# Optimization experiments

Measured on AMD Instinct MI355X. Metric: run time of the kernel, lower is better.

Reference implementation:

```python
import jax, jax.numpy as jnp
import numpy as np

EPS_BN = 1e-3   # nn.BatchNorm1d(eps=0.001)
LAMDA = 1e-5    # Point_Attentation.lamda


def _bn(x, g, b, m, v):
    # inference-mode BatchNorm1d over last dim
    return (x - m) * (g * jax.lax.rsqrt(v + EPS_BN)) + b


def _forward(features_low, features_high,
             bott_W, bott_b, bott_gamma, bott_beta, bott_mean, bott_var,
             qkv_W, qkv_gamma, qkv_beta, qkv_mean, qkv_var,
             mlp_W, mlp_gamma, mlp_beta, mlp_mean, mlp_var,
             fus_W, fus_b, fus_gamma, fus_beta, fus_mean, fus_var,
             batch_size):
    N, C = features_low.shape
    B = batch_size
    n = N // B  # points per batch segment (equal-length segments)

    # ---- Point_Attentation: per-point channel mean, var over channels / (n-1) ----
    x = features_low
    mean = jnp.mean(x, axis=-1, keepdims=True)
    d = x - mean
    var = jnp.sum(d * d, axis=-1, keepdims=True) / (n - 1)
    e_t = d * d / (4.0 * (var + LAMDA)) + 0.5
    x = x + jax.nn.sigmoid(e_t) * x

    for i in range(3):
        y = jax.nn.relu(_bn(x @ bott_W[2 * i] + bott_b[2 * i],
                            bott_gamma[2 * i], bott_beta[2 * i], bott_mean[2 * i], bott_var[2 * i]))
        y = jax.nn.relu(_bn(y @ bott_W[2 * i + 1] + bott_b[2 * i + 1],
                            bott_gamma[2 * i + 1], bott_beta[2 * i + 1], bott_mean[2 * i + 1], bott_var[2 * i + 1]))
        x = x + y

    # ---- fusion: per-batch QKV attention between low (x) and high features ----
    low = x.reshape(B, n, C)
    high = features_high.reshape(B, n, C)

    q = _bn(jnp.einsum('bnc,cd->bnd', low, qkv_W[0]), qkv_gamma[0], qkv_beta[0], qkv_mean[0], qkv_var[0])
    k = _bn(jnp.einsum('bnc,cd->bnd', high, qkv_W[1]), qkv_gamma[1], qkv_beta[1], qkv_mean[1], qkv_var[1])
    v = _bn(jnp.einsum('bnc,cd->bnd', high, qkv_W[2]), qkv_gamma[2], qkv_beta[2], qkv_mean[2], qkv_var[2])

    scale = 1.0 / jnp.sqrt(jnp.asarray(256.0, dtype=q.dtype))  # normal_dim = 256
    attn = jax.nn.softmax(jnp.einsum('bqc,bkc->bqk', q, k) * scale, axis=-1)
    ao = jnp.einsum('bqk,bkc->bqc', attn, v)

    # mlp: (Linear no-bias -> BN -> Dropout(eval=id) -> ReLU) x2
    h = jax.nn.relu(_bn(jnp.einsum('bnc,cd->bnd', ao, mlp_W[0]), mlp_gamma[0], mlp_beta[0], mlp_mean[0], mlp_var[0]))
    h = jax.nn.relu(_bn(jnp.einsum('bnc,cd->bnd', h, mlp_W[1]), mlp_gamma[1], mlp_beta[1], mlp_mean[1], mlp_var[1]))

    # linear_fusion: Linear(2C->C, bias) -> BN -> ReLU
    cat = jnp.concatenate([low, h], axis=-1)  # [B, n, 2C]
    out = jax.nn.relu(_bn(jnp.einsum('bnc,cd->bnd', cat, fus_W) + fus_b, fus_gamma, fus_beta, fus_mean, fus_var))
    return out.reshape(N, C)


def setup_inputs() -> dict:
    key = jax.random.key(0)
    ks = jax.random.split(key, 16)
    N, C, B = 16384, 256, 4
    s = 0.05
    d = {}
    d['features_low'] = jax.random.normal(ks[0], (N, C), jnp.float32)
    d['features_high'] = jax.random.normal(ks[1], (N, C), jnp.float32)
    d['bott_W'] = jax.random.normal(ks[2], (6, C, C), jnp.float32) * s
    d['bott_b'] = jnp.zeros((6, C), jnp.float32)
    d['bott_gamma'] = jnp.ones((6, C), jnp.float32)
    d['bott_beta'] = jnp.zeros((6, C), jnp.float32)
    d['bott_mean'] = jnp.zeros((6, C), jnp.float32)
    d['bott_var'] = jnp.ones((6, C), jnp.float32)
    d['qkv_W'] = jax.random.normal(ks[3], (3, C, C), jnp.float32) * s
    d['qkv_gamma'] = jnp.ones((3, C), jnp.float32)
    d['qkv_beta'] = jnp.zeros((3, C), jnp.float32)
    d['qkv_mean'] = jnp.zeros((3, C), jnp.float32)
    d['qkv_var'] = jnp.ones((3, C), jnp.float32)
    d['mlp_W'] = jax.random.normal(ks[4], (2, C, C), jnp.float32) * s
    d['mlp_gamma'] = jnp.ones((2, C), jnp.float32)
    d['mlp_beta'] = jnp.zeros((2, C), jnp.float32)
    d['mlp_mean'] = jnp.zeros((2, C), jnp.float32)
    d['mlp_var'] = jnp.ones((2, C), jnp.float32)
    d['fus_W'] = jax.random.normal(ks[5], (2 * C, C), jnp.float32) * s
    d['fus_b'] = jnp.zeros((C,), jnp.float32)
    d['fus_gamma'] = jnp.ones((C,), jnp.float32)
    d['fus_beta'] = jnp.zeros((C,), jnp.float32)
    d['fus_mean'] = jnp.zeros((C,), jnp.float32)
    d['fus_var'] = jnp.ones((C,), jnp.float32)
    d['batch_size'] = B
    return d


def reference(features_low, features_high,
              bott_W, bott_b, bott_gamma, bott_beta, bott_mean, bott_var,
              qkv_W, qkv_gamma, qkv_beta, qkv_mean, qkv_var,
              mlp_W, mlp_gamma, mlp_beta, mlp_mean, mlp_var,
              fus_W, fus_b, fus_gamma, fus_beta, fus_mean, fus_var,
              batch_size):
    return _forward(features_low, features_high,
                    bott_W, bott_b, bott_gamma, bott_beta, bott_mean, bott_var,
                    qkv_W, qkv_gamma, qkv_beta, qkv_mean, qkv_var,
                    mlp_W, mlp_gamma, mlp_beta, mlp_mean, mlp_var,
                    fus_W, fus_b, fus_gamma, fus_beta, fus_mean, fus_var,
                    batch_size)
```

## Files before the change

kernel.cpp:

```cpp
#include <hip/hip_runtime.h>
#include <cstdint>
#include <cstddef>

typedef float v4f __attribute__((ext_vector_type(4)));
typedef float v2f __attribute__((ext_vector_type(2)));
typedef short v8s __attribute__((ext_vector_type(8)));
typedef unsigned short v4u __attribute__((ext_vector_type(4)));

typedef unsigned short ubf;

#define NPTS 16384
#define CD   256
#define NBAT 4
#define NPB  4096

__device__ __forceinline__ float bf2f(ubf u) {
    union { unsigned u; float f; } c; c.u = ((unsigned)u) << 16; return c.f;
}
__device__ __forceinline__ ubf f2bf(float f) {
    union { float f; unsigned u; } c; c.f = f;
    unsigned u = c.u;
    u += 0x7fffu + ((u >> 16) & 1u);
    return (ubf)(u >> 16);
}

__global__ __launch_bounds__(256) void k_pre(
    const float* __restrict__ low, float* __restrict__ xout,
    const float* __restrict__ bott, const float* __restrict__ qkv,
    const float* __restrict__ mlp, const float* __restrict__ fus,
    ubf* __restrict__ wt) {
    const int bid = blockIdx.x;
    if (bid < 4096) {
        const int lane = threadIdx.x & 63;
        const int row  = bid * 4 + (threadIdx.x >> 6);
        const float* p = low + (size_t)row * CD + lane * 4;
        v4f v = *reinterpret_cast<const v4f*>(p);
        float d[4];
        float s = v[0] + v[1] + v[2] + v[3];
#pragma unroll
        for (int o = 32; o >= 1; o >>= 1) s += __shfl_xor(s, o);
        const float mean = s * (1.0f / 256.0f);
        float ss = 0.f;
#pragma unroll
        for (int i = 0; i < 4; ++i) { d[i] = v[i] - mean; ss += d[i] * d[i]; }
#pragma unroll
        for (int o = 32; o >= 1; o >>= 1) ss += __shfl_xor(ss, o);
        const float var = ss * (1.0f / 4095.0f);
        const float dn  = 1.0f / (4.0f * (var + 1e-5f));
        v4f o;
#pragma unroll
        for (int i = 0; i < 4; ++i) {
            const float e   = d[i] * d[i] * dn + 0.5f;
            const float sig = 1.0f / (1.0f + __expf(-e));
            o[i] = v[i] * (1.0f + sig);
        }
        *reinterpret_cast<v4f*>(xout + (size_t)row * CD + lane * 4) = o;
        return;
    }
    const int bid2 = bid - 4096;
    const int z = bid2 >> 7, r = bid2 & 127;
    const float* src; int K; size_t doff;
    if (z < 6)       { src = bott + (size_t)z * 65536;       K = 256; doff = (size_t)z * 65536; }
    else if (z < 9)  { src = qkv  + (size_t)(z - 6) * 65536; K = 256; doff = (size_t)z * 65536; }
    else if (z < 11) { src = mlp  + (size_t)(z - 9) * 65536; K = 256; doff = (size_t)z * 65536; }
    else             { src = fus;                            K = 512; doff = (size_t)11 * 65536; }
    const int kt = (r >> 3) * 32, nt = (r & 7) * 32;
    if (kt >= K) return;
    __shared__ ubf tile[32][33];
    const int tx = threadIdx.x & 31, ty = threadIdx.x >> 5;
#pragma unroll
    for (int i = 0; i < 4; ++i)
        tile[ty * 4 + i][tx] = f2bf(src[(size_t)(kt + ty * 4 + i) * 256 + nt + tx]);
    __syncthreads();
    ubf* dst = wt + doff;
#pragma unroll
    for (int i = 0; i < 4; ++i)
        dst[(size_t)(nt + ty * 4 + i) * K + kt + tx] = tile[tx][ty * 4 + i];
}

__global__ __launch_bounds__(256) void k_conv1(
    float* __restrict__ xA, const ubf* __restrict__ wT,
    const float* __restrict__ bb, const float* __restrict__ bg,
    const float* __restrict__ bbe, const float* __restrict__ bm_,
    const float* __restrict__ bv) {
    __shared__ __attribute__((aligned(16))) float xls[64 * 256];
    __shared__ __attribute__((aligned(16))) ubf   yls[64 * 256];

    const int lane = threadIdx.x & 63;
    const int w    = threadIdx.x >> 6;
    const int wr = w >> 1, wc = w & 1;
    const int q15 = lane & 15, g = lane >> 4;
    const int bm = blockIdx.x * 64;

    {
        float* xsrcb = xA + (size_t)bm * 256;
#pragma unroll
        for (int it = 0; it < 16; ++it) {
            const int L4 = (it * 256 + w * 64) * 4;
            const int Ll = L4 + lane * 4;
            const int row = Ll >> 8, col = (Ll & 255) ^ ((row & 7) << 3);
            __builtin_amdgcn_global_load_lds(
                (const __attribute__((address_space(1))) unsigned*)(xsrcb + row * 256 + col),
                (__attribute__((address_space(3))) unsigned*)(xls + L4), 16, 0, 0);
        }
    }
    __syncthreads();

    const int r0l = wr * 32 + q15;
#pragma unroll 1
    for (int s = 0; s < 3; ++s) {
        const ubf* W0 = wT + (size_t)(2 * s) * 65536;
        const ubf* W1 = wT + (size_t)(2 * s + 1) * 65536;

        v4f acc[2][8];
#pragma unroll
        for (int i = 0; i < 2; ++i)
#pragma unroll
            for (int j = 0; j < 8; ++j)
#pragma unroll
                for (int r = 0; r < 4; ++r) acc[i][j][r] = 0.f;
        for (int ks = 0; ks < 8; ++ks) {
            const int k0 = ks * 32 + g * 8;
            v8s afr[2], bfr[8];
#pragma unroll
            for (int mi = 0; mi < 2; ++mi) {
                const int row = r0l + mi * 16;
                const float* ap = &xls[row * 256 + (k0 ^ ((row & 7) << 3))];
                v4f a = *reinterpret_cast<const v4f*>(ap);
                v4f b = *reinterpret_cast<const v4f*>(ap + 4);
                v8s t;
#pragma unroll
                for (int j = 0; j < 4; ++j) { t[j] = (short)f2bf(a[j]); t[j + 4] = (short)f2bf(b[j]); }
                afr[mi] = t;
            }
#pragma unroll
            for (int ni = 0; ni < 8; ++ni)
                bfr[ni] = *reinterpret_cast<const v8s*>(W0 + (size_t)(wc * 128 + ni * 16 + q15) * 256 + k0);
#pragma unroll
            for (int mi = 0; mi < 2; ++mi)
#pragma unroll
                for (int ni = 0; ni < 8; ++ni)
                    acc[mi][ni] = __builtin_amdgcn_mfma_f32_16x16x32_bf16(afr[mi], bfr[ni], acc[mi][ni], 0, 0, 0);
        }
#pragma unroll
        for (int ni = 0; ni < 8; ++ni) {
            const int col = wc * 128 + ni * 16 + q15;
            const float sc  = bg[2 * s * 256 + col] * rsqrtf(bv[2 * s * 256 + col] + 1e-3f);
            const float tc  = bbe[2 * s * 256 + col] - bm_[2 * s * 256 + col] * sc;
            const float bia = bb[2 * s * 256 + col];
#pragma unroll
            for (int mi = 0; mi < 2; ++mi)
#pragma unroll
                for (int r = 0; r < 4; ++r) {
                    const int row = wr * 32 + mi * 16 + g * 4 + r;
                    float z = (acc[mi][ni][r] + bia) * sc + tc;
                    z = fmaxf(z, 0.f);
                    yls[row * 256 + (col ^ ((row & 7) << 3))] = f2bf(z);
                }
        }
        __syncthreads();

#pragma unroll
        for (int i = 0; i < 2; ++i)
#pragma unroll
            for (int j = 0; j < 8; ++j)
#pragma unroll
                for (int r = 0; r < 4; ++r) acc[i][j][r] = 0.f;
        for (int ks = 0; ks < 8; ++ks) {
            const int k0 = ks * 32 + g * 8;
            v8s afr[2], bfr[8];
#pragma unroll
            for (int mi = 0; mi < 2; ++mi) {
                const int row = r0l + mi * 16;
                afr[mi] = *reinterpret_cast<const v8s*>(&yls[row * 256 + (k0 ^ ((row & 7) << 3))]);
            }
#pragma unroll
            for (int ni = 0; ni < 8; ++ni)
                bfr[ni] = *reinterpret_cast<const v8s*>(W1 + (size_t)(wc * 128 + ni * 16 + q15) * 256 + k0);
#pragma unroll
            for (int mi = 0; mi < 2; ++mi)
#pragma unroll
                for (int ni = 0; ni < 8; ++ni)
                    acc[mi][ni] = __builtin_amdgcn_mfma_f32_16x16x32_bf16(afr[mi], bfr[ni], acc[mi][ni], 0, 0, 0);
        }
#pragma unroll
        for (int ni = 0; ni < 8; ++ni) {
            const int col = wc * 128 + ni * 16 + q15;
            const int c1 = (2 * s + 1) * 256 + col;
            const float sc  = bg[c1] * rsqrtf(bv[c1] + 1e-3f);
            const float tc  = bbe[c1] - bm_[c1] * sc;
            const float bia = bb[c1];
#pragma unroll
            for (int mi = 0; mi < 2; ++mi)
#pragma unroll
                for (int r = 0; r < 4; ++r) {
                    const int row = wr * 32 + mi * 16 + g * 4 + r;
                    float z = (acc[mi][ni][r] + bia) * sc + tc;
                    z = fmaxf(z, 0.f);
                    xls[row * 256 + (col ^ ((row & 7) << 3))] += z;
                }
        }
        __syncthreads();
    }

    {
        float* xdstb = xA + (size_t)bm * 256;
#pragma unroll
        for (int it = 0; it < 16; ++it) {
            const int Ll = (it * 256 + threadIdx.x) * 4;
            const int row = Ll >> 8, cl = Ll & 255;
            const int gcol = cl ^ ((row & 7) << 3);
            *reinterpret_cast<v4f*>(xdstb + row * 256 + gcol) =
                *reinterpret_cast<const v4f*>(xls + Ll);
        }
    }
}

__global__ __launch_bounds__(256) void k_qkv(
    const float* __restrict__ xA, const float* __restrict__ fh,
    const ubf* __restrict__ wTq,
    const float* __restrict__ qg, const float* __restrict__ qbe,
    const float* __restrict__ qm, const float* __restrict__ qv,
    ubf* __restrict__ qB, ubf* __restrict__ kB, ubf* __restrict__ vT) {
    const int m = blockIdx.y >> 1;
    const float* Af = (m == 0) ? xA : fh;
    const ubf* WT = wTq + m * 65536;
    const float* gamma = qg + m * 256;
    const float* beta  = qbe + m * 256;
    const float* bmean = qm + m * 256;
    const float* bvar  = qv + m * 256;

    const int lane = threadIdx.x & 63;
    const int w    = threadIdx.x >> 6;
    const int wr = w >> 1, wc = w & 1;
    const int q15 = lane & 15, g = lane >> 4;
    const int bm = blockIdx.x * 128, bn = (blockIdx.y & 1) * 128;
    const int r0 = bm + wr * 64 + q15;
    const int c0 = bn + wc * 64 + q15;

    v4f acc[4][4];
#pragma unroll
    for (int i = 0; i < 4; ++i)
#pragma unroll
        for (int j = 0; j < 4; ++j)
#pragma unroll
            for (int r = 0; r < 4; ++r) acc[i][j][r] = 0.f;

    for (int ks = 0; ks < 8; ++ks) {
        const int k0 = ks * 32 + g * 8;
        v8s afr[4], bfr[4];
#pragma unroll
        for (int mi = 0; mi < 4; ++mi) {
            const float* ap = Af + (size_t)(r0 + mi * 16) * CD + k0;
            v4f a = *reinterpret_cast<const v4f*>(ap);
            v4f b = *reinterpret_cast<const v4f*>(ap + 4);
            v8s t;
#pragma unroll
            for (int j = 0; j < 4; ++j) { t[j] = (short)f2bf(a[j]); t[j + 4] = (short)f2bf(b[j]); }
            afr[mi] = t;
        }
#pragma unroll
        for (int ni = 0; ni < 4; ++ni)
            bfr[ni] = *reinterpret_cast<const v8s*>(WT + (size_t)(c0 + ni * 16) * 256 + k0);
#pragma unroll
        for (int mi = 0; mi < 4; ++mi)
#pragma unroll
            for (int ni = 0; ni < 4; ++ni)
                acc[mi][ni] = __builtin_amdgcn_mfma_f32_16x16x32_bf16(afr[mi], bfr[ni], acc[mi][ni], 0, 0, 0);
    }

    ubf* outb = (m == 0) ? qB : kB;
#pragma unroll
    for (int ni = 0; ni < 4; ++ni) {
        const int col = c0 + ni * 16;
        const float sc = gamma[col] * rsqrtf(bvar[col] + 1e-3f);
        const float tc = beta[col] - bmean[col] * sc;
#pragma unroll
        for (int mi = 0; mi < 4; ++mi) {
            if (m == 2) {
                const int row0 = bm + wr * 64 + mi * 16 + g * 4;
                v4u pk;
#pragma unroll
                for (int r = 0; r < 4; ++r) pk[r] = f2bf(acc[mi][ni][r] * sc + tc);
                const int bb = row0 >> 12, key = row0 & 4095;
                *reinterpret_cast<v4u*>(vT + ((size_t)(bb * CD + col)) * NPB + key) = pk;
            } else {
#pragma unroll
                for (int r = 0; r < 4; ++r) {
                    const int row = bm + wr * 64 + mi * 16 + g * 4 + r;
                    outb[(size_t)row * CD + col] = f2bf(acc[mi][ni][r] * sc + tc);
                }
            }
        }
    }
}

__device__ __forceinline__ void stage_k256(const ubf* __restrict__ kg,
                                           ubf* kd, int wave, int lane) {
#pragma unroll
    for (int it = 0; it < 8; ++it) {
        const int Lb = it * 2048 + wave * 512;
        const int L  = Lb + lane * 8;
        const int key = L >> 8, c8 = (L & 255) ^ ((key & 7) << 3);
        __builtin_amdgcn_global_load_lds(
            (const __attribute__((address_space(1))) unsigned*)(kg + key * CD + c8),
            (__attribute__((address_space(3))) unsigned*)(kd + Lb), 16, 0, 0);
    }
}
__device__ __forceinline__ void stage_v256(const ubf* __restrict__ vg,
                                           ubf* vd, int wave, int lane) {
#pragma unroll
    for (int it = 0; it < 8; ++it) {
        const int Lb = it * 2048 + wave * 512;
        const int L  = Lb + lane * 8;
        const int c = L >> 6, k8 = (L & 63) ^ ((c & 7) << 3);
        __builtin_amdgcn_global_load_lds(
            (const __attribute__((address_space(1))) unsigned*)(vg + (size_t)c * NPB + k8),
            (__attribute__((address_space(3))) unsigned*)(vd + Lb), 16, 0, 0);
    }
}

__global__ __launch_bounds__(256) void k_attn(const ubf* __restrict__ qb, const ubf* __restrict__ kb,
                                              const ubf* __restrict__ vt,
                                              ubf* __restrict__ o0, ubf* __restrict__ o1,
                                              float* __restrict__ ml) {
    __shared__ __attribute__((aligned(16))) ubf kls[64 * 256];
    __shared__ __attribute__((aligned(16))) ubf vls[256 * 64];
    __shared__ __attribute__((aligned(16))) ubf pls[4 * 16 * 64];

    const int raw = blockIdx.x;
    const int xcd = raw & 7, qt = raw >> 3;
    const int b = xcd >> 1, half = xcd & 1;

    const int wave = threadIdx.x >> 6, lane = threadIdx.x & 63;
    const int q15 = lane & 15, g = lane >> 4;

    const ubf* qrow = qb + ((size_t)(b * NPB + qt * 64 + wave * 16 + q15)) * CD + g * 8;
    v8s qf[8];
#pragma unroll
    for (int cs = 0; cs < 8; ++cs) qf[cs] = *reinterpret_cast<const v8s*>(qrow + cs * 32);

    v4f oacc[16];
#pragma unroll
    for (int i = 0; i < 16; ++i)
#pragma unroll
        for (int r = 0; r < 4; ++r) oacc[i][r] = 0.f;
    float m_run = -3.0e38f, l_run = 0.f;

    const ubf* kgb = kb + ((size_t)(b * NPB) + half * 2048) * CD;
    const ubf* vgb = vt + (size_t)b * CD * NPB + half * 2048;
    ubf* pw = pls + wave * 1024;

    stage_k256(kgb, kls, wave, lane);
    __syncthreads();

    for (int kc = 0; kc < 32; ++kc) {
        stage_v256(vgb + kc * 64, vls, wave, lane);

        v4f sacc[4];
#pragma unroll
        for (int f = 0; f < 4; ++f)
#pragma unroll
            for (int r = 0; r < 4; ++r) sacc[f][r] = 0.f;
#pragma unroll
        for (int cs = 0; cs < 8; ++cs)
#pragma unroll
            for (int f = 0; f < 4; ++f) {
                const int key = 16 * f + q15;
                v8s af = *reinterpret_cast<const v8s*>(&kls[(key * CD + cs * 32 + g * 8) ^ ((key & 7) << 3)]);
                sacc[f] = __builtin_amdgcn_mfma_f32_16x16x32_bf16(af, qf[cs], sacc[f], 0, 0, 0);
            }

        __syncthreads();
        if (kc + 1 < 32)
            stage_k256(kgb + (size_t)(kc + 1) * 64 * CD, kls, wave, lane);

        float mloc = -3.0e38f;
#pragma unroll
        for (int f = 0; f < 4; ++f)
#pragma unroll
            for (int r = 0; r < 4; ++r) {
                float x = sacc[f][r] * 0.0625f;
                sacc[f][r] = x;
                mloc = fmaxf(mloc, x);
            }
        mloc = fmaxf(mloc, __shfl_xor(mloc, 16));
        mloc = fmaxf(mloc, __shfl_xor(mloc, 32));
        if (!__all(mloc <= m_run + 8.0f)) {
            const float mnew  = fmaxf(m_run, mloc);
            const float alpha = __expf(m_run - mnew);
            l_run *= alpha;
#pragma unroll
            for (int i = 0; i < 16; ++i)
#pragma unroll
                for (int r = 0; r < 4; ++r) oacc[i][r] *= alpha;
            m_run = mnew;
        }
        float lloc = 0.f;
#pragma unroll
        for (int f = 0; f < 4; ++f)
#pragma unroll
            for (int r = 0; r < 4; ++r) {
                float p = __expf(sacc[f][r] - m_run);
                sacc[f][r] = p;
                lloc += p;
            }
        lloc += __shfl_xor(lloc, 16);
        lloc += __shfl_xor(lloc, 32);
        l_run += lloc;

#pragma unroll
        for (int f = 0; f < 4; ++f) {
            unsigned u0, u1, u2, u3;
            { union { float f; unsigned u; } c; c.f = sacc[f][0]; u0 = c.u; }
            { union { float f; unsigned u; } c; c.f = sacc[f][1]; u1 = c.u; }
            { union { float f; unsigned u; } c; c.f = sacc[f][2]; u2 = c.u; }
            { union { float f; unsigned u; } c; c.f = sacc[f][3]; u3 = c.u; }
            unsigned p01 = (u0 >> 16) | (u1 & 0xFFFF0000u);
            unsigned p23 = (u2 >> 16) | (u3 & 0xFFFF0000u);
            const int e = q15 * 64 + 16 * f + 4 * g;
            *reinterpret_cast<unsigned*>(&pw[(e)     ^ ((q15 & 7) << 3)]) = p01;
            *reinterpret_cast<unsigned*>(&pw[(e + 2) ^ ((q15 & 7) << 3)]) = p23;
        }
        v8s pb0 = *reinterpret_cast<const v8s*>(&pw[(q15 * 64 +  0 + 8 * g) ^ ((q15 & 7) << 3)]);
        v8s pb1 = *reinterpret_cast<const v8s*>(&pw[(q15 * 64 + 32 + 8 * g) ^ ((q15 & 7) << 3)]);
#pragma unroll
        for (int mt = 0; mt < 16; ++mt) {
            const int c = 16 * mt + q15;
            v8s av0 = *reinterpret_cast<const v8s*>(&vls[(c * 64 +  0 + 8 * g) ^ ((c & 7) << 3)]);
            oacc[mt] = __builtin_amdgcn_mfma_f32_16x16x32_bf16(av0, pb0, oacc[mt], 0, 0, 0);
            v8s av1 = *reinterpret_cast<const v8s*>(&vls[(c * 64 + 32 + 8 * g) ^ ((c & 7) << 3)]);
            oacc[mt] = __builtin_amdgcn_mfma_f32_16x16x32_bf16(av1, pb1, oacc[mt], 0, 0, 0);
        }

        __syncthreads();
    }

    const int grow = b * NPB + qt * 64 + wave * 16 + q15;
    ubf* aor = (half ? o1 : o0) + (size_t)grow * CD;
#pragma unroll
    for (int mt = 0; mt < 16; ++mt) {
        v4u pk;
#pragma unroll
        for (int r = 0; r < 4; ++r) pk[r] = f2bf(oacc[mt][r]);
        *reinterpret_cast<v4u*>(aor + 16 * mt + 4 * g) = pk;
    }
    if (g == 0) {
        v2f d; d[0] = m_run; d[1] = l_run;
        *reinterpret_cast<v2f*>(ml + (size_t)(half * NPTS + grow) * 2) = d;
    }
}

__global__ __launch_bounds__(256) void k_tail(
    const ubf* __restrict__ o0, const ubf* __restrict__ o1, const float* __restrict__ ml,
    const float* __restrict__ xA, const ubf* __restrict__ wT,
    const float* __restrict__ mg, const float* __restrict__ mbe,
    const float* __restrict__ mm, const float* __restrict__ mv,
    const float* __restrict__ fb, const float* __restrict__ fg,
    const float* __restrict__ fbe, const float* __restrict__ fm,
    const float* __restrict__ fv, float* __restrict__ out) {
    __shared__ __attribute__((aligned(16))) ubf yls[64 * 256];

    const int lane = threadIdx.x & 63;
    const int w    = threadIdx.x >> 6;
    const int wr = w >> 1, wc = w & 1;
    const int q15 = lane & 15, g = lane >> 4;
    const int bm = blockIdx.x * 64;
    const int r0l = wr * 32 + q15;

    const ubf* W9  = wT + (size_t)9 * 65536;
    const ubf* W10 = wT + (size_t)10 * 65536;
    const ubf* W11 = wT + (size_t)11 * 65536;

    v4f acc[2][8];

    float a0[2], a1[2];
#pragma unroll
    for (int mi = 0; mi < 2; ++mi) {
        const int row = bm + r0l + mi * 16;
        const float m0 = ml[2 * row],          l0 = ml[2 * row + 1];
        const float m1 = ml[2 * (NPTS + row)], l1 = ml[2 * (NPTS + row) + 1];
        const float mx = fmaxf(m0, m1);
        const float w0 = __expf(m0 - mx), w1 = __expf(m1 - mx);
        const float inv = 1.0f / (w0 * l0 + w1 * l1);
        a0[mi] = w0 * inv; a1[mi] = w1 * inv;
    }
#pragma unroll
    for (int i = 0; i < 2; ++i)
#pragma unroll
        for (int j = 0; j < 8; ++j)
#pragma unroll
            for (int r = 0; r < 4; ++r) acc[i][j][r] = 0.f;
    for (int ks = 0; ks < 8; ++ks) {
        const int k0 = ks * 32 + g * 8;
        v8s afr[2], bfr[8];
#pragma unroll
        for (int mi = 0; mi < 2; ++mi) {
            const int row = bm + r0l + mi * 16;
            v8s u0 = *reinterpret_cast<const v8s*>(o0 + (size_t)row * CD + k0);
            v8s u1 = *reinterpret_cast<const v8s*>(o1 + (size_t)row * CD + k0);
            v8s t;
#pragma unroll
            for (int j = 0; j < 8; ++j)
                t[j] = (short)f2bf(a0[mi] * bf2f((ubf)u0[j]) + a1[mi] * bf2f((ubf)u1[j]));
            afr[mi] = t;
        }
#pragma unroll
        for (int ni = 0; ni < 8; ++ni)
            bfr[ni] = *reinterpret_cast<const v8s*>(W9 + (size_t)(wc * 128 + ni * 16 + q15) * 256 + k0);
#pragma unroll
        for (int mi = 0; mi < 2; ++mi)
#pragma unroll
            for (int ni = 0; ni < 8; ++ni)
                acc[mi][ni] = __builtin_amdgcn_mfma_f32_16x16x32_bf16(afr[mi], bfr[ni], acc[mi][ni], 0, 0, 0);
    }
#pragma unroll
    for (int ni = 0; ni < 8; ++ni) {
        const int col = wc * 128 + ni * 16 + q15;
        const float sc = mg[col] * rsqrtf(mv[col] + 1e-3f);
        const float tc = mbe[col] - mm[col] * sc;
#pragma unroll
        for (int mi = 0; mi < 2; ++mi)
#pragma unroll
            for (int r = 0; r < 4; ++r) {
                const int row = wr * 32 + mi * 16 + g * 4 + r;
                float z = fmaxf(acc[mi][ni][r] * sc + tc, 0.f);
                yls[row * 256 + (col ^ ((row & 7) << 3))] = f2bf(z);
            }
    }
    __syncthreads();

#pragma unroll
    for (int i = 0; i < 2; ++i)
#pragma unroll
        for (int j = 0; j < 8; ++j)
#pragma unroll
            for (int r = 0; r < 4; ++r) acc[i][j][r] = 0.f;
    for (int ks = 0; ks < 8; ++ks) {
        const int k0 = ks * 32 + g * 8;
        v8s afr[2], bfr[8];
#pragma unroll
        for (int mi = 0; mi < 2; ++mi) {
            const int row = r0l + mi * 16;
            afr[mi] = *reinterpret_cast<const v8s*>(&yls[row * 256 + (k0 ^ ((row & 7) << 3))]);
        }
#pragma unroll
        for (int ni = 0; ni < 8; ++ni)
            bfr[ni] = *reinterpret_cast<const v8s*>(W10 + (size_t)(wc * 128 + ni * 16 + q15) * 256 + k0);
#pragma unroll
        for (int mi = 0; mi < 2; ++mi)
#pragma unroll
            for (int ni = 0; ni < 8; ++ni)
                acc[mi][ni] = __builtin_amdgcn_mfma_f32_16x16x32_bf16(afr[mi], bfr[ni], acc[mi][ni], 0, 0, 0);
    }
    __syncthreads();
#pragma unroll
    for (int ni = 0; ni < 8; ++ni) {
        const int col = wc * 128 + ni * 16 + q15;
        const float sc = mg[256 + col] * rsqrtf(mv[256 + col] + 1e-3f);
        const float tc = mbe[256 + col] - mm[256 + col] * sc;
#pragma unroll
        for (int mi = 0; mi < 2; ++mi)
#pragma unroll
            for (int r = 0; r < 4; ++r) {
                const int row = wr * 32 + mi * 16 + g * 4 + r;
                float z = fmaxf(acc[mi][ni][r] * sc + tc, 0.f);
                yls[row * 256 + (col ^ ((row & 7) << 3))] = f2bf(z);
            }
    }
    __syncthreads();

#pragma unroll
    for (int i = 0; i < 2; ++i)
#pragma unroll
        for (int j = 0; j < 8; ++j)
#pragma unroll
            for (int r = 0; r < 4; ++r) acc[i][j][r] = 0.f;
    for (int ks = 0; ks < 16; ++ks) {
        const int k0 = ks * 32 + g * 8;
        v8s afr[2], bfr[8];
#pragma unroll
        for (int mi = 0; mi < 2; ++mi) {
            if (k0 < 256) {
                const float* ap = xA + (size_t)(bm + r0l + mi * 16) * CD + k0;
                v4f a = *reinterpret_cast<const v4f*>(ap);
                v4f b = *reinterpret_cast<const v4f*>(ap + 4);
                v8s t;
#pragma unroll
                for (int j = 0; j < 4; ++j) { t[j] = (short)f2bf(a[j]); t[j + 4] = (short)f2bf(b[j]); }
                afr[mi] = t;
            } else {
                const int row = r0l + mi * 16, kk = k0 - 256;
                afr[mi] = *reinterpret_cast<const v8s*>(&yls[row * 256 + (kk ^ ((row & 7) << 3))]);
            }
        }
#pragma unroll
        for (int ni = 0; ni < 8; ++ni)
            bfr[ni] = *reinterpret_cast<const v8s*>(W11 + (size_t)(wc * 128 + ni * 16 + q15) * 512 + k0);
#pragma unroll
        for (int mi = 0; mi < 2; ++mi)
#pragma unroll
            for (int ni = 0; ni < 8; ++ni)
                acc[mi][ni] = __builtin_amdgcn_mfma_f32_16x16x32_bf16(afr[mi], bfr[ni], acc[mi][ni], 0, 0, 0);
    }
#pragma unroll
    for (int ni = 0; ni < 8; ++ni) {
        const int col = wc * 128 + ni * 16 + q15;
        const float sc = fg[col] * rsqrtf(fv[col] + 1e-3f);
        const float tc = fbe[col] - fm[col] * sc;
        const float bia = fb[col];
#pragma unroll
        for (int mi = 0; mi < 2; ++mi)
#pragma unroll
            for (int r = 0; r < 4; ++r) {
                const int row = bm + wr * 32 + mi * 16 + g * 4 + r;
                float z = fmaxf((acc[mi][ni][r] + bia) * sc + tc, 0.f);
                out[(size_t)row * CD + col] = z;
            }
    }
}

extern "C" void kernel_launch(void* const* d_in, const int* in_sizes, int n_in,
                              void* d_out, int out_size, void* d_ws, size_t ws_size,
                              hipStream_t stream) {
    const float* f_low   = (const float*)d_in[0];
    const float* f_high  = (const float*)d_in[1];
    const float* bott_W  = (const float*)d_in[2];
    const float* bott_b  = (const float*)d_in[3];
    const float* bott_g  = (const float*)d_in[4];
    const float* bott_be = (const float*)d_in[5];
    const float* bott_m  = (const float*)d_in[6];
    const float* bott_v  = (const float*)d_in[7];
    const float* qkv_W   = (const float*)d_in[8];
    const float* qkv_g   = (const float*)d_in[9];
    const float* qkv_be  = (const float*)d_in[10];
    const float* qkv_m   = (const float*)d_in[11];
    const float* qkv_v   = (const float*)d_in[12];
    const float* mlp_W   = (const float*)d_in[13];
    const float* mlp_g   = (const float*)d_in[14];
    const float* mlp_be  = (const float*)d_in[15];
    const float* mlp_m   = (const float*)d_in[16];
    const float* mlp_v   = (const float*)d_in[17];
    const float* fus_W   = (const float*)d_in[18];
    const float* fus_b   = (const float*)d_in[19];
    const float* fus_g   = (const float*)d_in[20];
    const float* fus_be  = (const float*)d_in[21];
    const float* fus_m   = (const float*)d_in[22];
    const float* fus_v   = (const float*)d_in[23];
    (void)in_sizes; (void)n_in; (void)out_size; (void)ws_size;

    char* ws = (char*)d_ws;
    const size_t MB = 1024 * 1024;
    float* xA = (float*)(ws);
    ubf*   o0 = (ubf*)  (ws + 17 * MB);
    ubf*   qB = (ubf*)  (ws + 26 * MB);
    ubf*   kB = (ubf*)  (ws + 35 * MB);
    ubf*   vT = (ubf*)  (ws + 44 * MB);
    ubf*   wT = (ubf*)  (ws + 53 * MB);
    ubf*   o1 = (ubf*)  (ws + 56 * MB);
    float* ml = (float*)(ws + 65 * MB);

    k_pre<<<dim3(4096 + 1536), dim3(256), 0, stream>>>(f_low, xA,
                                                       bott_W, qkv_W, mlp_W, fus_W, wT);

    k_conv1<<<dim3(256), dim3(256), 0, stream>>>(xA, wT,
                                                 bott_b, bott_g, bott_be, bott_m, bott_v);

    k_qkv<<<dim3(128, 6), dim3(256), 0, stream>>>(xA, f_high, wT + (size_t)6 * 65536,
                                                  qkv_g, qkv_be, qkv_m, qkv_v, qB, kB, vT);

    k_attn<<<dim3(512), dim3(256), 0, stream>>>(qB, kB, vT, o0, o1, ml);

    k_tail<<<dim3(256), dim3(256), 0, stream>>>(o0, o1, ml, xA, wT,
                                                mlp_g, mlp_be, mlp_m, mlp_v,
                                                fus_b, fus_g, fus_be, fus_m, fus_v,
                                                (float*)d_out);
}
```

Measured before the change: 305.3 us.

## Merge conv1 with K/V projection, split Q projection, double attention query tile

The bottleneck stack and the K/V projections now share one heterogeneous launch. Conv1 uses 32-row tiles over 512 blocks, and the remaining 512 blocks compute K and V from features_high, which does not depend on conv1. Q projection becomes its own kernel. The attention kernel now gives each wave two 16-row query sub-tiles, halving grid size and reusing each staged K/V tile across twice as many queries, at the cost of higher register pressure (launch_bounds 256,1).

```diff
diff --git a/kernel.cpp b/kernel.cpp
--- a/kernel.cpp
+++ b/kernel.cpp
@@ -78,165 +78,208 @@
         dst[(size_t)(nt + ty * 4 + i) * K + kt + tx] = tile[tx][ty * 4 + i];
 }
 
-__global__ __launch_bounds__(256) void k_conv1(
-    float* __restrict__ xA, const ubf* __restrict__ wT,
+__global__ __launch_bounds__(256) void k_mid(
+    float* __restrict__ xA, const float* __restrict__ fh, const ubf* __restrict__ wT,
     const float* __restrict__ bb, const float* __restrict__ bg,
     const float* __restrict__ bbe, const float* __restrict__ bm_,
-    const float* __restrict__ bv) {
-    __shared__ __attribute__((aligned(16))) float xls[64 * 256];
-    __shared__ __attribute__((aligned(16))) ubf   yls[64 * 256];
+    const float* __restrict__ bv,
+    const float* __restrict__ qg, const float* __restrict__ qbe,
+    const float* __restrict__ qm, const float* __restrict__ qv,
+    ubf* __restrict__ kB, ubf* __restrict__ vT) {
+    __shared__ __attribute__((aligned(16))) float xls[32 * 256];
+    __shared__ __attribute__((aligned(16))) ubf   yls[32 * 256];
 
     const int lane = threadIdx.x & 63;
     const int w    = threadIdx.x >> 6;
     const int wr = w >> 1, wc = w & 1;
     const int q15 = lane & 15, g = lane >> 4;
-    const int bm = blockIdx.x * 64;
-
-    {
-        float* xsrcb = xA + (size_t)bm * 256;
-#pragma unroll
-        for (int it = 0; it < 16; ++it) {
-            const int L4 = (it * 256 + w * 64) * 4;
-            const int Ll = L4 + lane * 4;
-            const int row = Ll >> 8, col = (Ll & 255) ^ ((row & 7) << 3);
-            __builtin_amdgcn_global_load_lds(
-                (const __attribute__((address_space(1))) unsigned*)(xsrcb + row * 256 + col),
-                (__attribute__((address_space(3))) unsigned*)(xls + L4), 16, 0, 0);
-        }
-    }
-    __syncthreads();
-
-    const int r0l = wr * 32 + q15;
+    const int bid = blockIdx.x;
+
+    if (bid < 512) {
+        const int bm = bid * 32;
+        {
+            float* xsrcb = xA + (size_t)bm * 256;
+#pragma unroll
+            for (int it = 0; it < 8; ++it) {
+                const int L4 = (it * 256 + w * 64) * 4;
+                const int Ll = L4 + lane * 4;
+                const int row = Ll >> 8, col = (Ll & 255) ^ ((row & 7) << 3);
+                __builtin_amdgcn_global_load_lds(
+                    (const __attribute__((address_space(1))) unsigned*)(xsrcb + row * 256 + col),
+                    (__attribute__((address_space(3))) unsigned*)(xls + L4), 16, 0, 0);
+            }
+        }
+        __syncthreads();
+
+        const int r0l = wr * 16 + q15;
 #pragma unroll 1
-    for (int s = 0; s < 3; ++s) {
-        const ubf* W0 = wT + (size_t)(2 * s) * 65536;
-        const ubf* W1 = wT + (size_t)(2 * s + 1) * 65536;
-
-        v4f acc[2][8];
-#pragma unroll
-        for (int i = 0; i < 2; ++i)
+        for (int s = 0; s < 3; ++s) {
+            const ubf* W0 = wT + (size_t)(2 * s) * 65536;
+            const ubf* W1 = wT + (size_t)(2 * s + 1) * 65536;
+
+            v4f acc[8];
 #pragma unroll
             for (int j = 0; j < 8; ++j)
 #pragma unroll
-                for (int r = 0; r < 4; ++r) acc[i][j][r] = 0.f;
-        for (int ks = 0; ks < 8; ++ks) {
-            const int k0 = ks * 32 + g * 8;
-            v8s afr[2], bfr[8];
-#pragma unroll
-            for (int mi = 0; mi < 2; ++mi) {
-                const int row = r0l + mi * 16;
-                const float* ap = &xls[row * 256 + (k0 ^ ((row & 7) << 3))];
+                for (int r = 0; r < 4; ++r) acc[j][r] = 0.f;
+            for (int ks = 0; ks < 8; ++ks) {
+                const int k0 = ks * 32 + g * 8;
+                const float* ap = &xls[r0l * 256 + (k0 ^ ((r0l & 7) << 3))];
                 v4f a = *reinterpret_cast<const v4f*>(ap);
                 v4f b = *reinterpret_cast<const v4f*>(ap + 4);
-                v8s t;
-#pragma unroll
-                for (int j = 0; j < 4; ++j) { t[j] = (short)f2bf(a[j]); t[j + 4] = (short)f2bf(b[j]); }
-                afr[mi] = t;
-            }
-#pragma unroll
-            for (int ni = 0; ni < 8; ++ni)
-                bfr[ni] = *reinterpret_cast<const v8s*>(W0 + (size_t)(wc * 128 + ni * 16 + q15) * 256 + k0);
-#pragma unroll
-            for (int mi = 0; mi < 2; ++mi)
+                v8s afr;
+#pragma unroll
+                for (int j = 0; j < 4; ++j) { afr[j] = (short)f2bf(a[j]); afr[j + 4] = (short)f2bf(b[j]); }
+                v8s bfr[8];
 #pragma unroll
                 for (int ni = 0; ni < 8; ++ni)
-                    acc[mi][ni] = __builtin_amdgcn_mfma_f32_16x16x32_bf16(afr[mi], bfr[ni], acc[mi][ni], 0, 0, 0);
-        }
-#pragma unroll
-        for (int ni = 0; ni < 8; ++ni) {
-            const int col = wc * 128 + ni * 16 + q15;
-            const float sc  = bg[2 * s * 256 + col] * rsqrtf(bv[2 * s * 256 + col] + 1e-3f);
-            const float tc  = bbe[2 * s * 256 + col] - bm_[2 * s * 256 + col] * sc;
-            const float bia = bb[2 * s * 256 + col];
-#pragma unroll
-            for (int mi = 0; mi < 2; ++mi)
+                    bfr[ni] = *reinterpret_cast<const v8s*>(W0 + (size_t)(wc * 128 + ni * 16 + q15) * 256 + k0);
+#pragma unroll
+                for (int ni = 0; ni < 8; ++ni)
+                    acc[ni] = __builtin_amdgcn_mfma_f32_16x16x32_bf16(afr, bfr[ni], acc[ni], 0, 0, 0);
+            }
+#pragma unroll
+            for (int ni = 0; ni < 8; ++ni) {
+                const int col = wc * 128 + ni * 16 + q15;
+                const int c0i = 2 * s * 256 + col;
+                const float sc  = bg[c0i] * rsqrtf(bv[c0i] + 1e-3f);
+                const float tc  = bbe[c0i] - bm_[c0i] * sc;
+                const float bia = bb[c0i];
 #pragma unroll
                 for (int r = 0; r < 4; ++r) {
-                    const int row = wr * 32 + mi * 16 + g * 4 + r;
-                    float z = (acc[mi][ni][r] + bia) * sc + tc;
-                    z = fmaxf(z, 0.f);
+                    const int row = wr * 16 + g * 4 + r;
+                    float z = fmaxf((acc[ni][r] + bia) * sc + tc, 0.f);
                     yls[row * 256 + (col ^ ((row & 7) << 3))] = f2bf(z);
                 }
-        }
-        __syncthreads();
-
-#pragma unroll
-        for (int i = 0; i < 2; ++i)
+            }
+            __syncthreads();
+
 #pragma unroll
             for (int j = 0; j < 8; ++j)
 #pragma unroll
-                for (int r = 0; r < 4; ++r) acc[i][j][r] = 0.f;
-        for (int ks = 0; ks < 8; ++ks) {
-            const int k0 = ks * 32 + g * 8;
-            v8s afr[2], bfr[8];
-#pragma unroll
-            for (int mi = 0; mi < 2; ++mi) {
-                const int row = r0l + mi * 16;
-                afr[mi] = *reinterpret_cast<const v8s*>(&yls[row * 256 + (k0 ^ ((row & 7) << 3))]);
-            }
-#pragma unroll
-            for (int ni = 0; ni < 8; ++ni)
-                bfr[ni] = *reinterpret_cast<const v8s*>(W1 + (size_t)(wc * 128 + ni * 16 + q15) * 256 + k0);
-#pragma unroll
-            for (int mi = 0; mi < 2; ++mi)
+                for (int r = 0; r < 4; ++r) acc[j][r] = 0.f;
+            for (int ks = 0; ks < 8; ++ks) {
+                const int k0 = ks * 32 + g * 8;
+                v8s afr = *reinterpret_cast<const v8s*>(&yls[r0l * 256 + (k0 ^ ((r0l & 7) << 3))]);
+                v8s bfr[8];
 #pragma unroll
                 for (int ni = 0; ni < 8; ++ni)
-                    acc[mi][ni] = __builtin_amdgcn_mfma_f32_16x16x32_bf16(afr[mi], bfr[ni], acc[mi][ni], 0, 0, 0);
-        }
-#pragma unroll
-        for (int ni = 0; ni < 8; ++ni) {
-            const int col = wc * 128 + ni * 16 + q15;
-            const int c1 = (2 * s + 1) * 256 + col;
-            const float sc  = bg[c1] * rsqrtf(bv[c1] + 1e-3f);
-            const float tc  = bbe[c1] - bm_[c1] * sc;
-            const float bia = bb[c1];
-#pragma unroll
-            for (int mi = 0; mi < 2; ++mi)
+                    bfr[ni] = *reinterpret_cast<const v8s*>(W1 + (size_t)(wc * 128 + ni * 16 + q15) * 256 + k0);
+#pragma unroll
+                for (int ni = 0; ni < 8; ++ni)
+                    acc[ni] = __builtin_amdgcn_mfma_f32_16x16x32_bf16(afr, bfr[ni], acc[ni], 0, 0, 0);
+            }
+#pragma unroll
+            for (int ni = 0; ni < 8; ++ni) {
+                const int col = wc * 128 + ni * 16 + q15;
+                const int c1i = (2 * s + 1) * 256 + col;
+                const float sc  = bg[c1i] * rsqrtf(bv[c1i] + 1e-3f);
+                const float tc  = bbe[c1i] - bm_[c1i] * sc;
+                const float bia = bb[c1i];
 #pragma unroll
                 for (int r = 0; r < 4; ++r) {
-                    const int row = wr * 32 + mi * 16 + g * 4 + r;
-                    float z = (acc[mi][ni][r] + bia) * sc + tc;
-                    z = fmaxf(z, 0.f);
+                    const int row = wr * 16 + g * 4 + r;
+                    float z = fmaxf((acc[ni][r] + bia) * sc + tc, 0.f);
                     xls[row * 256 + (col ^ ((row & 7) << 3))] += z;
                 }
-        }
-        __syncthreads();
-    }
-
-    {
-        float* xdstb = xA + (size_t)bm * 256;
-#pragma unroll
-        for (int it = 0; it < 16; ++it) {
-            const int Ll = (it * 256 + threadIdx.x) * 4;
-            const int row = Ll >> 8, cl = Ll & 255;
-            const int gcol = cl ^ ((row & 7) << 3);
-            *reinterpret_cast<v4f*>(xdstb + row * 256 + gcol) =
-                *reinterpret_cast<const v4f*>(xls + Ll);
-        }
-    }
-}
-
-__global__ __launch_bounds__(256) void k_qkv(
-    const float* __restrict__ xA, const float* __restrict__ fh,
-    const ubf* __restrict__ wTq,
+            }
+            __syncthreads();
+        }
+
+        {
+            float* xdstb = xA + (size_t)bm * 256;
+#pragma unroll
+            for (int it = 0; it < 8; ++it) {
+                const int Ll = (it * 256 + threadIdx.x) * 4;
+                const int row = Ll >> 8, cl = Ll & 255;
+                *reinterpret_cast<v4f*>(xdstb + row * 256 + (cl ^ ((row & 7) << 3))) =
+                    *reinterpret_cast<const v4f*>(xls + Ll);
+            }
+        }
+        return;
+    }
+
+    const int bid2 = bid - 512;
+    const int m = bid2 >> 8;
+    const int sub = bid2 & 255;
+    const int bm = (sub >> 1) * 128, bn = (sub & 1) * 128;
+    const ubf* WT = wT + (size_t)(7 + m) * 65536;
+    const float* gamma = qg  + (1 + m) * 256;
+    const float* beta  = qbe + (1 + m) * 256;
+    const float* bmean = qm  + (1 + m) * 256;
+    const float* bvar  = qv  + (1 + m) * 256;
+    const int r0 = bm + wr * 64 + q15;
+    const int c0 = bn + wc * 64 + q15;
+
+    v4f acc[4][4];
+#pragma unroll
+    for (int i = 0; i < 4; ++i)
+#pragma unroll
+        for (int j = 0; j < 4; ++j)
+#pragma unroll
+            for (int r = 0; r < 4; ++r) acc[i][j][r] = 0.f;
+
+    for (int ks = 0; ks < 8; ++ks) {
+        const int k0 = ks * 32 + g * 8;
+        v8s afr[4], bfr[4];
+#pragma unroll
+        for (int mi = 0; mi < 4; ++mi) {
+            const float* ap = fh + (size_t)(r0 + mi * 16) * CD + k0;
+            v4f a = *reinterpret_cast<const v4f*>(ap);
+            v4f b = *reinterpret_cast<const v4f*>(ap + 4);
+            v8s t;
+#pragma unroll
+            for (int j = 0; j < 4; ++j) { t[j] = (short)f2bf(a[j]); t[j + 4] = (short)f2bf(b[j]); }
+            afr[mi] = t;
+        }
+#pragma unroll
+        for (int ni = 0; ni < 4; ++ni)
+            bfr[ni] = *reinterpret_cast<const v8s*>(WT + (size_t)(c0 + ni * 16) * 256 + k0);
+#pragma unroll
+        for (int mi = 0; mi < 4; ++mi)
+#pragma unroll
+            for (int ni = 0; ni < 4; ++ni)
+                acc[mi][ni] = __builtin_amdgcn_mfma_f32_16x16x32_bf16(afr[mi], bfr[ni], acc[mi][ni], 0, 0, 0);
+    }
+
+#pragma unroll
+    for (int ni = 0; ni < 4; ++ni) {
+        const int col = c0 + ni * 16;
+        const float sc = gamma[col] * rsqrtf(bvar[col] + 1e-3f);
+        const float tc = beta[col] - bmean[col] * sc;
+#pragma unroll
+        for (int mi = 0; mi < 4; ++mi) {
+            if (m == 1) {
+                const int row0 = bm + wr * 64 + mi * 16 + g * 4;
+                v4u pk;
+#pragma unroll
+                for (int r = 0; r < 4; ++r) pk[r] = f2bf(acc[mi][ni][r] * sc + tc);
+                const int bb2 = row0 >> 12, key = row0 & 4095;
+                *reinterpret_cast<v4u*>(vT + ((size_t)(bb2 * CD + col)) * NPB + key) = pk;
+            } else {
+#pragma unroll
+                for (int r = 0; r < 4; ++r) {
+                    const int row = bm + wr * 64 + mi * 16 + g * 4 + r;
+                    kB[(size_t)row * CD + col] = f2bf(acc[mi][ni][r] * sc + tc);
+                }
+            }
+        }
+    }
+}
+
+__global__ __launch_bounds__(256) void k_qproj(
+    const float* __restrict__ xA, const ubf* __restrict__ wT,
     const float* __restrict__ qg, const float* __restrict__ qbe,
     const float* __restrict__ qm, const float* __restrict__ qv,
-    ubf* __restrict__ qB, ubf* __restrict__ kB, ubf* __restrict__ vT) {
-    const int m = blockIdx.y >> 1;
-    const float* Af = (m == 0) ? xA : fh;
-    const ubf* WT = wTq + m * 65536;
-    const float* gamma = qg + m * 256;
-    const float* beta  = qbe + m * 256;
-    const float* bmean = qm + m * 256;
-    const float* bvar  = qv + m * 256;
-
+    ubf* __restrict__ qB) {
     const int lane = threadIdx.x & 63;
     const int w    = threadIdx.x >> 6;
     const int wr = w >> 1, wc = w & 1;
     const int q15 = lane & 15, g = lane >> 4;
-    const int bm = blockIdx.x * 128, bn = (blockIdx.y & 1) * 128;
+    const int bm = blockIdx.x * 128, bn = blockIdx.y * 128;
     const int r0 = bm + wr * 64 + q15;
     const int c0 = bn + wc * 64 + q15;
+    const ubf* WT = wT + (size_t)6 * 65536;
 
     v4f acc[4][4];
 #pragma unroll
@@ -251,7 +294,7 @@
         v8s afr[4], bfr[4];
 #pragma unroll
         for (int mi = 0; mi < 4; ++mi) {
-            const float* ap = Af + (size_t)(r0 + mi * 16) * CD + k0;
+            const float* ap = xA + (size_t)(r0 + mi * 16) * CD + k0;
             v4f a = *reinterpret_cast<const v4f*>(ap);
             v4f b = *reinterpret_cast<const v4f*>(ap + 4);
             v8s t;
@@ -269,29 +312,18 @@
                 acc[mi][ni] = __builtin_amdgcn_mfma_f32_16x16x32_bf16(afr[mi], bfr[ni], acc[mi][ni], 0, 0, 0);
     }
 
-    ubf* outb = (m == 0) ? qB : kB;
 #pragma unroll
     for (int ni = 0; ni < 4; ++ni) {
         const int col = c0 + ni * 16;
-        const float sc = gamma[col] * rsqrtf(bvar[col] + 1e-3f);
-        const float tc = beta[col] - bmean[col] * sc;
-#pragma unroll
-        for (int mi = 0; mi < 4; ++mi) {
-            if (m == 2) {
-                const int row0 = bm + wr * 64 + mi * 16 + g * 4;
-                v4u pk;
-#pragma unroll
-                for (int r = 0; r < 4; ++r) pk[r] = f2bf(acc[mi][ni][r] * sc + tc);
-                const int bb = row0 >> 12, key = row0 & 4095;
-                *reinterpret_cast<v4u*>(vT + ((size_t)(bb * CD + col)) * NPB + key) = pk;
-            } else {
-#pragma unroll
-                for (int r = 0; r < 4; ++r) {
-                    const int row = bm + wr * 64 + mi * 16 + g * 4 + r;
-                    outb[(size_t)row * CD + col] = f2bf(acc[mi][ni][r] * sc + tc);
-                }
-            }
-        }
+        const float sc = qg[col] * rsqrtf(qv[col] + 1e-3f);
+        const float tc = qbe[col] - qm[col] * sc;
+#pragma unroll
+        for (int mi = 0; mi < 4; ++mi)
+#pragma unroll
+            for (int r = 0; r < 4; ++r) {
+                const int row = bm + wr * 64 + mi * 16 + g * 4 + r;
+                qB[(size_t)row * CD + col] = f2bf(acc[mi][ni][r] * sc + tc);
+            }
     }
 }
 
@@ -320,13 +352,13 @@
     }
 }
 
-__global__ __launch_bounds__(256) void k_attn(const ubf* __restrict__ qb, const ubf* __restrict__ kb,
-                                              const ubf* __restrict__ vt,
-                                              ubf* __restrict__ o0, ubf* __restrict__ o1,
-                                              float* __restrict__ ml) {
+__global__ __launch_bounds__(256, 1) void k_attn(const ubf* __restrict__ qb, const ubf* __restrict__ kb,
+                                                 const ubf* __restrict__ vt,
+                                                 ubf* __restrict__ o0, ubf* __restrict__ o1,
+                                                 float* __restrict__ ml) {
     __shared__ __attribute__((aligned(16))) ubf kls[64 * 256];
     __shared__ __attribute__((aligned(16))) ubf vls[256 * 64];
-    __shared__ __attribute__((aligned(16))) ubf pls[4 * 16 * 64];
+    __shared__ __attribute__((aligned(16))) ubf pls[4 * 2 * 1024];
 
     const int raw = blockIdx.x;
     const int xcd = raw & 7, qt = raw >> 3;
@@ -334,22 +366,28 @@
 
     const int wave = threadIdx.x >> 6, lane = threadIdx.x & 63;
     const int q15 = lane & 15, g = lane >> 4;
-
-    const ubf* qrow = qb + ((size_t)(b * NPB + qt * 64 + wave * 16 + q15)) * CD + g * 8;
-    v8s qf[8];
-#pragma unroll
-    for (int cs = 0; cs < 8; ++cs) qf[cs] = *reinterpret_cast<const v8s*>(qrow + cs * 32);
-
-    v4f oacc[16];
-#pragma unroll
-    for (int i = 0; i < 16; ++i)
-#pragma unroll
-        for (int r = 0; r < 4; ++r) oacc[i][r] = 0.f;
-    float m_run = -3.0e38f, l_run = 0.f;
+    const int swzP = (q15 & 7) << 3;
+
+    v8s qf[2][8];
+#pragma unroll
+    for (int s = 0; s < 2; ++s) {
+        const ubf* qrow = qb + ((size_t)(b * NPB + qt * 128 + wave * 32 + s * 16 + q15)) * CD + g * 8;
+#pragma unroll
+        for (int cs = 0; cs < 8; ++cs) qf[s][cs] = *reinterpret_cast<const v8s*>(qrow + cs * 32);
+    }
+
+    v4f oacc[2][16];
+#pragma unroll
+    for (int s = 0; s < 2; ++s)
+#pragma unroll
+        for (int i = 0; i < 16; ++i)
+#pragma unroll
+            for (int r = 0; r < 4; ++r) oacc[s][i][r] = 0.f;
+    float m_run[2] = { -3.0e38f, -3.0e38f }, l_run[2] = { 0.f, 0.f };
 
     const ubf* kgb = kb + ((size_t)(b * NPB) + half * 2048) * CD;
     const ubf* vgb = vt + (size_t)b * CD * NPB + half * 2048;
-    ubf* pw = pls + wave * 1024;
+    ubf* pw = pls + wave * 2048;
 
     stage_k256(kgb, kls, wave, lane);
     __syncthreads();
@@ -357,97 +395,113 @@
     for (int kc = 0; kc < 32; ++kc) {
         stage_v256(vgb + kc * 64, vls, wave, lane);
 
-        v4f sacc[4];
-#pragma unroll
-        for (int f = 0; f < 4; ++f)
-#pragma unroll
-            for (int r = 0; r < 4; ++r) sacc[f][r] = 0.f;
+        v4f sacc[2][4];
+#pragma unroll
+        for (int s = 0; s < 2; ++s)
+#pragma unroll
+            for (int f = 0; f < 4; ++f)
+#pragma unroll
+                for (int r = 0; r < 4; ++r) sacc[s][f][r] = 0.f;
 #pragma unroll
         for (int cs = 0; cs < 8; ++cs)
 #pragma unroll
             for (int f = 0; f < 4; ++f) {
                 const int key = 16 * f + q15;
                 v8s af = *reinterpret_cast<const v8s*>(&kls[(key * CD + cs * 32 + g * 8) ^ ((key & 7) << 3)]);
-                sacc[f] = __builtin_amdgcn_mfma_f32_16x16x32_bf16(af, qf[cs], sacc[f], 0, 0, 0);
+                sacc[0][f] = __builtin_amdgcn_mfma_f32_16x16x32_bf16(af, qf[0][cs], sacc[0][f], 0, 0, 0);
+                sacc[1][f] = __builtin_amdgcn_mfma_f32_16x16x32_bf16(af, qf[1][cs], sacc[1][f], 0, 0, 0);
             }
 
         __syncthreads();
         if (kc + 1 < 32)
             stage_k256(kgb + (size_t)(kc + 1) * 64 * CD, kls, wave, lane);
 
-        float mloc = -3.0e38f;
-#pragma unroll
-        for (int f = 0; f < 4; ++f)
-#pragma unroll
-            for (int r = 0; r < 4; ++r) {
-                float x = sacc[f][r] * 0.0625f;
-                sacc[f][r] = x;
-                mloc = fmaxf(mloc, x);
-            }
-        mloc = fmaxf(mloc, __shfl_xor(mloc, 16));
-        mloc = fmaxf(mloc, __shfl_xor(mloc, 32));
-        if (!__all(mloc <= m_run + 8.0f)) {
-            const float mnew  = fmaxf(m_run, mloc);
-            const float alpha = __expf(m_run - mnew);
-            l_run *= alpha;
-#pragma unroll
-            for (int i = 0; i < 16; ++i)
-#pragma unroll
-                for (int r = 0; r < 4; ++r) oacc[i][r] *= alpha;
-            m_run = mnew;
-        }
-        float lloc = 0.f;
-#pragma unroll
-        for (int f = 0; f < 4; ++f)
-#pragma unroll
-            for (int r = 0; r < 4; ++r) {
-                float p = __expf(sacc[f][r] - m_run);
-                sacc[f][r] = p;
-                lloc += p;
-            }
-        lloc += __shfl_xor(lloc, 16);
-        lloc += __shfl_xor(lloc, 32);
-        l_run += lloc;
-
-#pragma unroll
-        for (int f = 0; f < 4; ++f) {
-            unsigned u0, u1, u2, u3;
-            { union { float f; unsigned u; } c; c.f = sacc[f][0]; u0 = c.u; }
-            { union { float f; unsigned u; } c; c.f = sacc[f][1]; u1 = c.u; }
-            { union { float f; unsigned u; } c; c.f = sacc[f][2]; u2 = c.u; }
-            { union { float f; unsigned u; } c; c.f = sacc[f][3]; u3 = c.u; }
-            unsigned p01 = (u0 >> 16) | (u1 & 0xFFFF0000u);
-            unsigned p23 = (u2 >> 16) | (u3 & 0xFFFF0000u);
-            const int e = q15 * 64 + 16 * f + 4 * g;
-            *reinterpret_cast<unsigned*>(&pw[(e)     ^ ((q15 & 7) << 3)]) = p01;
-            *reinterpret_cast<unsigned*>(&pw[(e + 2) ^ ((q15 & 7) << 3)]) = p23;
-        }
-        v8s pb0 = *reinterpret_cast<const v8s*>(&pw[(q15 * 64 +  0 + 8 * g) ^ ((q15 & 7) << 3)]);
-        v8s pb1 = *reinterpret_cast<const v8s*>(&pw[(q15 * 64 + 32 + 8 * g) ^ ((q15 & 7) << 3)]);
+#pragma unroll
+        for (int s = 0; s < 2; ++s) {
+            float mloc = -3.0e38f;
+#pragma unroll
+            for (int f = 0; f < 4; ++f)
+#pragma unroll
+                for (int r = 0; r < 4; ++r) {
+                    float x = sacc[s][f][r] * 0.0625f;
+                    sacc[s][f][r] = x;
+                    mloc = fmaxf(mloc, x);
+                }
+            mloc = fmaxf(mloc, __shfl_xor(mloc, 16));
+            mloc = fmaxf(mloc, __shfl_xor(mloc, 32));
+            if (!__all(mloc <= m_run[s] + 8.0f)) {
+                const float mnew  = fmaxf(m_run[s], mloc);
+                const float alpha = __expf(m_run[s] - mnew);
+                l_run[s] *= alpha;
+#pragma unroll
+                for (int i = 0; i < 16; ++i)
+#pragma unroll
+                    for (int r = 0; r < 4; ++r) oacc[s][i][r] *= alpha;
+                m_run[s] = mnew;
+            }
+            float lloc = 0.f;
+#pragma unroll
+            for (int f = 0; f < 4; ++f)
+#pragma unroll
+                for (int r = 0; r < 4; ++r) {
+                    float p = __expf(sacc[s][f][r] - m_run[s]);
+                    sacc[s][f][r] = p;
+                    lloc += p;
+                }
+            lloc += __shfl_xor(lloc, 16);
+            lloc += __shfl_xor(lloc, 32);
+            l_run[s] += lloc;
+
+#pragma unroll
+            for (int f = 0; f < 4; ++f) {
+                unsigned u0, u1, u2, u3;
+                { union { float f; unsigned u; } c; c.f = sacc[s][f][0]; u0 = c.u; }
+                { union { float f; unsigned u; } c; c.f = sacc[s][f][1]; u1 = c.u; }
+                { union { float f; unsigned u; } c; c.f = sacc[s][f][2]; u2 = c.u; }
+                { union { float f; unsigned u; } c; c.f = sacc[s][f][3]; u3 = c.u; }
+                unsigned p01 = (u0 >> 16) | (u1 & 0xFFFF0000u);
+                unsigned p23 = (u2 >> 16) | (u3 & 0xFFFF0000u);
+                const int e = s * 1024 + q15 * 64 + 16 * f + 4 * g;
+                *reinterpret_cast<unsigned*>(&pw[(e)     ^ swzP]) = p01;
+                *reinterpret_cast<unsigned*>(&pw[(e + 2) ^ swzP]) = p23;
+            }
+        }
+
+        v8s pb0[2], pb1[2];
+#pragma unroll
+        for (int s = 0; s < 2; ++s) {
+            pb0[s] = *reinterpret_cast<const v8s*>(&pw[(s * 1024 + q15 * 64 +  0 + 8 * g) ^ swzP]);
+            pb1[s] = *reinterpret_cast<const v8s*>(&pw[(s * 1024 + q15 * 64 + 32 + 8 * g) ^ swzP]);
+        }
 #pragma unroll
         for (int mt = 0; mt < 16; ++mt) {
             const int c = 16 * mt + q15;
             v8s av0 = *reinterpret_cast<const v8s*>(&vls[(c * 64 +  0 + 8 * g) ^ ((c & 7) << 3)]);
-            oacc[mt] = __builtin_amdgcn_mfma_f32_16x16x32_bf16(av0, pb0, oacc[mt], 0, 0, 0);
+            oacc[0][mt] = __builtin_amdgcn_mfma_f32_16x16x32_bf16(av0, pb0[0], oacc[0][mt], 0, 0, 0);
+            oacc[1][mt] = __builtin_amdgcn_mfma_f32_16x16x32_bf16(av0, pb0[1], oacc[1][mt], 0, 0, 0);
             v8s av1 = *reinterpret_cast<const v8s*>(&vls[(c * 64 + 32 + 8 * g) ^ ((c & 7) << 3)]);
-            oacc[mt] = __builtin_amdgcn_mfma_f32_16x16x32_bf16(av1, pb1, oacc[mt], 0, 0, 0);
+            oacc[0][mt] = __builtin_amdgcn_mfma_f32_16x16x32_bf16(av1, pb1[0], oacc[0][mt], 0, 0, 0);
+            oacc[1][mt] = __builtin_amdgcn_mfma_f32_16x16x32_bf16(av1, pb1[1], oacc[1][mt], 0, 0, 0);
         }
 
         __syncthreads();
     }
 
-    const int grow = b * NPB + qt * 64 + wave * 16 + q15;
-    ubf* aor = (half ? o1 : o0) + (size_t)grow * CD;
-#pragma unroll
-    for (int mt = 0; mt < 16; ++mt) {
-        v4u pk;
-#pragma unroll
-        for (int r = 0; r < 4; ++r) pk[r] = f2bf(oacc[mt][r]);
-        *reinterpret_cast<v4u*>(aor + 16 * mt + 4 * g) = pk;
-    }
-    if (g == 0) {
-        v2f d; d[0] = m_run; d[1] = l_run;
-        *reinterpret_cast<v2f*>(ml + (size_t)(half * NPTS + grow) * 2) = d;
+#pragma unroll
+    for (int s = 0; s < 2; ++s) {
+        const int grow = b * NPB + qt * 128 + wave * 32 + s * 16 + q15;
+        ubf* aor = (half ? o1 : o0) + (size_t)grow * CD;
+#pragma unroll
+        for (int mt = 0; mt < 16; ++mt) {
+            v4u pk;
+#pragma unroll
+            for (int r = 0; r < 4; ++r) pk[r] = f2bf(oacc[s][mt][r]);
+            *reinterpret_cast<v4u*>(aor + 16 * mt + 4 * g) = pk;
+        }
+        if (g == 0) {
+            v2f d; d[0] = m_run[s]; d[1] = l_run[s];
+            *reinterpret_cast<v2f*>(ml + (size_t)(half * NPTS + grow) * 2) = d;
+        }
     }
 }
 
@@ -663,13 +717,13 @@
     k_pre<<<dim3(4096 + 1536), dim3(256), 0, stream>>>(f_low, xA,
                                                        bott_W, qkv_W, mlp_W, fus_W, wT);
 
-    k_conv1<<<dim3(256), dim3(256), 0, stream>>>(xA, wT,
-                                                 bott_b, bott_g, bott_be, bott_m, bott_v);
-
-    k_qkv<<<dim3(128, 6), dim3(256), 0, stream>>>(xA, f_high, wT + (size_t)6 * 65536,
-                                                  qkv_g, qkv_be, qkv_m, qkv_v, qB, kB, vT);
-
-    k_attn<<<dim3(512), dim3(256), 0, stream>>>(qB, kB, vT, o0, o1, ml);
+    k_mid<<<dim3(1024), dim3(256), 0, stream>>>(xA, f_high, wT,
+                                                bott_b, bott_g, bott_be, bott_m, bott_v,
+                                                qkv_g, qkv_be, qkv_m, qkv_v, kB, vT);
+
+    k_qproj<<<dim3(128, 2), dim3(256), 0, stream>>>(xA, wT, qkv_g, qkv_be, qkv_m, qkv_v, qB);
+
+    k_attn<<<dim3(256), dim3(256), 0, stream>>>(qB, kB, vT, o0, o1, ml);
 
     k_tail<<<dim3(256), dim3(256), 0, stream>>>(o0, o1, ml, xA, wT,
                                                 mlp_g, mlp_be, mlp_m, mlp_v,
```

Measured after the change: 354.0 us. +15.9%, slower.
